# Kernel tuning notes

Measured on AMD Instinct MI355X. Metric: run time of the kernel, lower is better.

Reference implementation:

```python
import jax, jax.numpy as jnp
import numpy as np

N_EMBD = 1024
HEAD_SIZE = 64
B, T = 8, 4096


def setup_inputs() -> dict:
    key = jax.random.key(0)
    kx, kk, kq, kv = jax.random.split(key, 4)
    scale = 1.0 / np.sqrt(N_EMBD)
    x = jax.random.normal(kx, (B, T, N_EMBD), dtype=jnp.float32)
    # nn.Linear(N_EMBD, head_size, bias=False) weights, stored as [in, out] for x @ W
    W_k = jax.random.uniform(kk, (N_EMBD, HEAD_SIZE), dtype=jnp.float32, minval=-scale, maxval=scale)
    W_q = jax.random.uniform(kq, (N_EMBD, HEAD_SIZE), dtype=jnp.float32, minval=-scale, maxval=scale)
    W_v = jax.random.uniform(kv, (N_EMBD, HEAD_SIZE), dtype=jnp.float32, minval=-scale, maxval=scale)
    return {"x": x, "W_k": W_k, "W_q": W_q, "W_v": W_v}


def reference(x, W_k, W_q, W_v) -> jnp.ndarray:
    # x: [B,T,E]; projections to [B,T,H]
    k = jnp.einsum("bte,eh->bth", x, W_k)
    q = jnp.einsum("bte,eh->bth", x, W_q)
    v = jnp.einsum("bte,eh->bth", x, W_v)
    H = W_k.shape[1]
    scores = jnp.einsum("bth,bsh->bts", q, k) * (H ** -0.5)  # [B,T,T]
    Tlen = x.shape[1]
    causal = jnp.tril(jnp.ones((Tlen, Tlen), dtype=bool))
    scores = jnp.where(causal, scores, -jnp.inf)
    attn = jax.nn.softmax(scores, axis=-1)
    # dropout is identity in eval mode (deterministic reference)
    return jnp.einsum("bts,bsh->bth", attn, v)
```

## Files before the change

### kernel.cpp

```cpp
#include <hip/hip_runtime.h>
#include <hip/hip_bf16.h>
#include <math.h>


#define BB 8
#define TT 4096
#define EE 1024
#define HH 64
#define NSLOT 160
#define SLOTF 4160

typedef __attribute__((ext_vector_type(8))) short short8;
typedef __attribute__((ext_vector_type(4))) float floatx4;
typedef short8 __attribute__((may_alias)) short8_a;
typedef uint2 __attribute__((may_alias)) uint2_a;
typedef uint4 __attribute__((may_alias)) uint4_a;
typedef float4 __attribute__((may_alias)) float4_a;

#define GLDS(gp, lp)                                                     \
  __builtin_amdgcn_global_load_lds(                                      \
      (const __attribute__((address_space(1))) unsigned int*)(gp),       \
      (__attribute__((address_space(3))) unsigned int*)(lp), 16, 0, 0)

__device__ __forceinline__ unsigned short f2bf(float f) {
  union { float f; unsigned int u; } v; v.f = f;
  unsigned int r = v.u + 0x7fffu + ((v.u >> 16) & 1u);
  return (unsigned short)(r >> 16);
}
__device__ __forceinline__ unsigned int pk2(float a, float b) {
  unsigned int r;
  asm("v_cvt_pk_bf16_f32 %0, %1, %2" : "=v"(r) : "v"(a), "v"(b));
  return r;
}
__device__ __forceinline__ floatx4 fzero() {
  floatx4 z = {0.f, 0.f, 0.f, 0.f};
  return z;
}
__device__ __forceinline__ floatx4 mfma_bf16(short8 a, short8 b, floatx4 c) {
  return __builtin_amdgcn_mfma_f32_16x16x32_bf16(a, b, c, 0, 0, 0);
}
__device__ __forceinline__ short8 pack8(float4 a, float4 b) {
  union { unsigned int u[4]; short8 s; } r;
  r.u[0] = pk2(a.x, a.y);
  r.u[1] = pk2(a.z, a.w);
  r.u[2] = pk2(b.x, b.y);
  r.u[3] = pk2(b.z, b.w);
  return r.s;
}

__global__ __launch_bounds__(256) void wt_kernel(
    const float* __restrict__ Wk, const float* __restrict__ Wq,
    const float* __restrict__ Wv, unsigned short* __restrict__ wt3) {
  __shared__ float tile[64][65];
  const int m = blockIdx.y;
  const int eb = blockIdx.x;
  const float* W = (m == 0) ? Wk : ((m == 1) ? Wq : Wv);
  const int t = threadIdx.x;
  {
    const int r = t >> 2;
    const int c0 = (t & 3) * 16;
    const float* src = W + (size_t)(eb * 64 + r) * 64 + c0;
#pragma unroll
    for (int i = 0; i < 16; ++i) tile[r][c0 + i] = src[i];
  }
  __syncthreads();
  {
    const int h = t >> 2;
    const int e0 = (t & 3) * 16;
    unsigned int w[8];
#pragma unroll
    for (int i = 0; i < 8; ++i)
      w[i] = pk2(tile[e0 + 2 * i][h], tile[e0 + 2 * i + 1][h]);
    unsigned short* dst = wt3 + (size_t)(m * 64 + h) * EE + eb * 64 + e0;
    ((uint4_a*)dst)[0] = make_uint4(w[0], w[1], w[2], w[3]);
    ((uint4_a*)(dst + 8))[0] = make_uint4(w[4], w[5], w[6], w[7]);
  }
}

__global__ __launch_bounds__(256) void proj_kernel(
    const float* __restrict__ x, const unsigned short* __restrict__ wt3,
    unsigned short* __restrict__ kws, unsigned short* __restrict__ qws,
    unsigned short* __restrict__ vtws) {
  __shared__ __align__(16) unsigned char LB[3][20480];
  const int t = threadIdx.x;
  const int wv = t >> 6, lane = t & 63;
  const int l16 = lane & 15, quad = lane >> 4;
  const int mshalf = wv & 1;
  const int jbase = (wv >> 1) * 6;
  const size_t row0 = (size_t)blockIdx.x * 64;

  floatx4 acc[6][2];
#pragma unroll
  for (int j = 0; j < 6; ++j)
#pragma unroll
    for (int m2 = 0; m2 < 2; ++m2) acc[j][m2] = fzero();

  const int sg = (lane & 7) ^ ((lane >> 3) & 7);
  const int arow = lane >> 3;

#define STAGE(bufp, cc)                                                        \
  {                                                                            \
    _Pragma("unroll") for (int i = 0; i < 5; ++i) {                            \
      const int q = wv * 5 + i;                                                \
      if (q < 8) {                                                             \
        const float* gp =                                                      \
            x + (row0 + 8 * q + arow) * EE + (cc) * 32 + sg * 4;               \
        GLDS(gp, (bufp) + q * 1024);                                           \
      } else {                                                                 \
        const int j = q - 8;                                                   \
        const unsigned short* gp =                                             \
            wt3 + (size_t)(j * 16 + l16) * EE + (cc) * 32 + quad * 8;          \
        GLDS(gp, (bufp) + 8192 + j * 1024);                                    \
      }                                                                        \
    }                                                                          \
  }

  STAGE(&LB[0][0], 0);
  STAGE(&LB[1][0], 1);
  asm volatile("s_waitcnt vmcnt(5)" ::: "memory");
  __builtin_amdgcn_s_barrier();
  __builtin_amdgcn_sched_barrier(0);

  int cur = 0;
  for (int c = 0; c < 32; ++c) {
    const unsigned char* Ab = &LB[cur][0];
    float4 a4[2][2];
#pragma unroll
    for (int m2 = 0; m2 < 2; ++m2) {
      const int row = mshalf * 32 + m2 * 16 + l16;
#pragma unroll
      for (int h = 0; h < 2; ++h) {
        const int gsw = (quad * 2 + h) ^ (row & 7);
        a4[m2][h] = *(const float4_a*)(Ab + row * 128 + gsw * 16);
      }
    }
    if (c + 2 < 32) {
      int sb = cur + 2;
      if (sb >= 3) sb -= 3;
      STAGE(&LB[sb][0], c + 2);
    }
    short8 af[2];
#pragma unroll
    for (int m2 = 0; m2 < 2; ++m2) af[m2] = pack8(a4[m2][0], a4[m2][1]);
#pragma unroll
    for (int jj = 0; jj < 6; ++jj) {
      short8 bfv = *(const short8_a*)(Ab + 8192 + (size_t)(jbase + jj) * 1024 +
                                      lane * 16);
#pragma unroll
      for (int m2 = 0; m2 < 2; ++m2)
        acc[jj][m2] = mfma_bf16(af[m2], bfv, acc[jj][m2]);
    }
    if (c < 31) {
      if (c <= 29) {
        asm volatile("s_waitcnt vmcnt(5)" ::: "memory");
      } else {
        asm volatile("s_waitcnt vmcnt(0)" ::: "memory");
      }
      __builtin_amdgcn_s_barrier();
      __builtin_amdgcn_sched_barrier(0);
    }
    cur = (cur == 2) ? 0 : cur + 1;
  }
#undef STAGE

  const int b = (int)(row0 >> 12);
  const int tt0 = (int)(row0 & (TT - 1));
#pragma unroll
  for (int j = 0; j < 6; ++j) {
    const int jg = jbase + j;
    const int m = jg >> 2;
    const int h0 = (jg & 3) * 16;
#pragma unroll
    for (int m2 = 0; m2 < 2; ++m2) {
      floatx4 a = acc[j][m2];
      const int rbase = mshalf * 32 + m2 * 16 + quad * 4;
      if (m == 0) {
#pragma unroll
        for (int r = 0; r < 4; ++r)
          kws[(row0 + rbase + r) * HH + h0 + l16] = f2bf(a[r]);
      } else if (m == 1) {
#pragma unroll
        for (int r = 0; r < 4; ++r)
          qws[(row0 + rbase + r) * HH + h0 + l16] = f2bf(a[r] * 0.18033688011112042f);
      } else {
        uint2 p;
        p.x = pk2(a[0], a[1]);
        p.y = pk2(a[2], a[3]);
        ((uint2_a*)&vtws[(size_t)(b * 64 + h0 + l16) * TT + tt0 + rbase])[0] = p;
      }
    }
  }
}

template <bool SPLIT>
__global__ __launch_bounds__(256) void attn_kernel(
    const unsigned short* __restrict__ kws, const unsigned short* __restrict__ qws,
    const unsigned short* __restrict__ vtws, float* __restrict__ dst) {
  __shared__ unsigned short KV[2][16][512];
  __shared__ unsigned short pb[4][16][72];
  const int t = threadIdx.x;
  const int wv = t >> 6, lane = t & 63;
  const int l16 = lane & 15, quad = lane >> 4;
  const int id = (int)blockIdx.x;
  int b, jq, kt0, kt1;
  if (SPLIT) {
    b = id & 7;
    const int cid = id >> 3;
    int s, S;
    if (cid < 16) {
      jq = cid; s = 0; S = 1;
    } else if (cid < 48) {
      const int u = cid - 16; jq = 16 + (u >> 1); s = u & 1; S = 2;
    } else if (cid < 96) {
      const int u = cid - 48; const int d = u / 3; jq = 32 + d; s = u - 3 * d; S = 3;
    } else {
      const int u = cid - 96; jq = 48 + (u >> 2); s = u & 3; S = 4;
    }
    const int n = jq + 1;
    kt0 = (s * n) / S;
    kt1 = ((s + 1) * n) / S;
  } else {
    const int r255 = id & 255;
    b = r255 & 7;
    const int m = r255 >> 3;
    jq = (id < 256) ? m : 63 - m;
    kt0 = 0;
    kt1 = jq + 1;
  }
  const int q0 = jq * 64;
  const int qrow = q0 + wv * 16 + l16;

  const unsigned short* qp = qws + ((size_t)b * TT + qrow) * HH + quad * 8;
  short8 qa0 = *(const short8_a*)(qp);
  short8 qa1 = *(const short8_a*)(qp + 32);

  floatx4 o[4];
#pragma unroll
  for (int nt = 0; nt < 4; ++nt) o[nt] = fzero();
  float lsum = 0.f;

#define STAGE_KV(buf, ks)                                                      \
  {                                                                            \
    _Pragma("unroll") for (int i = 0; i < 4; ++i) {                            \
      const int idx = wv * 4 + i;                                              \
      const unsigned short* gp;                                                \
      if (idx < 8) {                                                           \
        const int nt = idx >> 1, f = idx & 1;                                  \
        gp = kws + ((size_t)b * TT + (ks) + nt * 16 + l16) * HH + f * 32 +     \
             quad * 8;                                                         \
      } else {                                                                 \
        const int nt = (idx - 8) >> 1, f = idx & 1;                            \
        gp = vtws + ((size_t)(b * 64 + nt * 16 + l16)) * TT + (ks) + f * 32 +  \
             quad * 8;                                                         \
      }                                                                        \
      GLDS(gp, &KV[buf][idx][0]);                                              \
    }                                                                          \
  }

  STAGE_KV(0, kt0 * 64);
  __syncthreads();

  for (int kt = kt0; kt < kt1; ++kt) {
    const int cur = (kt - kt0) & 1;
    const int ks = kt * 64;
    if (kt + 1 < kt1) STAGE_KV(cur ^ 1, ks + 64);

    floatx4 sc[4];
#pragma unroll
    for (int nt = 0; nt < 4; ++nt) {
      short8 kf0 = *(const short8_a*)&KV[cur][nt * 2][lane * 8];
      short8 kf1 = *(const short8_a*)&KV[cur][nt * 2 + 1][lane * 8];
      floatx4 z = fzero();
      z = mfma_bf16(kf0, qa0, z);
      z = mfma_bf16(kf1, qa1, z);
      sc[nt] = z;
    }
    if (kt == jq) {
#pragma unroll
      for (int nt = 0; nt < 4; ++nt)
#pragma unroll
        for (int r = 0; r < 4; ++r) {
          const int key = ks + nt * 16 + quad * 4 + r;
          if (key > qrow) sc[nt][r] = -1e30f;
        }
    }
#pragma unroll
    for (int nt = 0; nt < 4; ++nt) {
      const float p0 = exp2f(sc[nt][0]);
      const float p1 = exp2f(sc[nt][1]);
      const float p2 = exp2f(sc[nt][2]);
      const float p3 = exp2f(sc[nt][3]);
      lsum += (p0 + p1) + (p2 + p3);
      uint2 pw;
      pw.x = pk2(p0, p1);
      pw.y = pk2(p2, p3);
      ((uint2_a*)&pb[wv][l16][nt * 16 + quad * 4])[0] = pw;
    }
    short8 pf0 = *(const short8_a*)&pb[wv][l16][quad * 8];
    short8 pf1 = *(const short8_a*)&pb[wv][l16][quad * 8 + 32];
#pragma unroll
    for (int nt = 0; nt < 4; ++nt) {
      short8 vf0 = *(const short8_a*)&KV[cur][8 + nt * 2][lane * 8];
      short8 vf1 = *(const short8_a*)&KV[cur][8 + nt * 2 + 1][lane * 8];
      o[nt] = mfma_bf16(vf0, pf0, o[nt]);
      o[nt] = mfma_bf16(vf1, pf1, o[nt]);
    }
    __syncthreads();
  }
#undef STAGE_KV

  float lr = lsum;
  lr += __shfl_xor(lr, 16);
  lr += __shfl_xor(lr, 32);

  if (SPLIT) {
    float* op = dst + (size_t)id * SLOTF;
    const int ql = wv * 16 + l16;
#pragma unroll
    for (int nt = 0; nt < 4; ++nt) {
      float4 st;
      st.x = o[nt][0];
      st.y = o[nt][1];
      st.z = o[nt][2];
      st.w = o[nt][3];
      *(float4_a*)&op[(size_t)ql * 64 + nt * 16 + quad * 4] = st;
    }
    if (lane < 16) op[4096 + wv * 16 + lane] = lr;
  } else {
    const float inv = 1.0f / lr;
#pragma unroll
    for (int nt = 0; nt < 4; ++nt) {
      float4 st;
      st.x = o[nt][0] * inv;
      st.y = o[nt][1] * inv;
      st.z = o[nt][2] * inv;
      st.w = o[nt][3] * inv;
      *(float4_a*)&dst[((size_t)b * TT + qrow) * HH + nt * 16 + quad * 4] = st;
    }
  }
}

__global__ __launch_bounds__(256) void comb_kernel(
    const float* __restrict__ part, float* __restrict__ out) {
  const int id = (int)blockIdx.x;
  const int b = id & 7;
  const int jq = id >> 3;
  const int tq = jq >> 4;
  const int S = tq + 1;
  const int P = 8 * tq * (tq + 1) + (jq & 15) * S;
  const int t = threadIdx.x;
  const int r0 = t >> 6;
  const int h = t & 63;
  const float* s0 = part + (size_t)(b + 8 * P) * SLOTF;
  const size_t sstr = (size_t)8 * SLOTF;

#pragma unroll 4
  for (int i = 0; i < 16; ++i) {
    const int r = i * 4 + r0;
    float acc = 0.f, l = 0.f;
    for (int s2 = 0; s2 < S; ++s2) {
      acc += s0[(size_t)s2 * sstr + (size_t)r * 64 + h];
      l += s0[(size_t)s2 * sstr + 4096 + r];
    }
    out[((size_t)b * TT + jq * 64 + r) * HH + h] = acc / l;
  }
}

extern "C" void kernel_launch(void* const* d_in, const int* in_sizes, int n_in,
                              void* d_out, int out_size, void* d_ws, size_t ws_size,
                              hipStream_t stream) {
  const float* x = (const float*)d_in[0];
  const float* Wk = (const float*)d_in[1];
  const float* Wq = (const float*)d_in[2];
  const float* Wv = (const float*)d_in[3];
  float* out = (float*)d_out;

  unsigned short* kws = (unsigned short*)d_ws;
  unsigned short* qws = kws + (size_t)BB * TT * HH;
  unsigned short* vtws = qws + (size_t)BB * TT * HH;
  unsigned short* wt3 = vtws + (size_t)BB * TT * HH;
  float* part = (float*)(wt3 + (size_t)3 * HH * EE);

  const size_t base_bytes = (size_t)3 * BB * TT * HH * 2 + (size_t)3 * HH * EE * 2;
  const size_t need = base_bytes + (size_t)BB * NSLOT * SLOTF * 4;
  const bool use_split = (ws_size >= need);

  hipLaunchKernelGGL(wt_kernel, dim3(16, 3), dim3(256), 0, stream, Wk, Wq, Wv, wt3);
  hipLaunchKernelGGL(proj_kernel, dim3(512), dim3(256), 0, stream, x, wt3, kws, qws,
                     vtws);
  if (use_split) {
    hipLaunchKernelGGL((attn_kernel<true>), dim3(BB * NSLOT), dim3(256), 0, stream,
                       kws, qws, vtws, part);
    hipLaunchKernelGGL(comb_kernel, dim3(512), dim3(256), 0, stream, part, out);
  } else {
    hipLaunchKernelGGL((attn_kernel<false>), dim3(512), dim3(256), 0, stream,
                       kws, qws, vtws, out);
  }
}
```

Before: 283.3 us.

## Use 128-row query tiles with 8-wave blocks in split attention

Replaces the 4-wave, 64-query-row split attention kernel with an 8-wave, 128-query-row variant. Each staged K/V tile is now shared by twice as many query rows, which halves K/V global traffic and the number of staging loads per row. The split schedule drops to 80 slots per batch, and the combine kernel is adjusted to 128-row groups. In exchange there are fewer blocks, so the causal work balances more coarsely, and two diagonal tiles per block need masking.

Measured after the change: 297.2 us. 1.05x slower.

```diff
diff --git a/kernel.cpp b/kernel.cpp
--- a/kernel.cpp
+++ b/kernel.cpp
@@ -7,8 +7,8 @@
 #define TT 4096
 #define EE 1024
 #define HH 64
-#define NSLOT 160
-#define SLOTF 4160
+#define NSLOT2 80
+#define SLOTF2 8320
 
 typedef __attribute__((ext_vector_type(8))) short short8;
 typedef __attribute__((ext_vector_type(4))) float floatx4;
@@ -192,7 +192,131 @@
   }
 }
 
-template <bool SPLIT>
+__global__ __launch_bounds__(512) void attn8_kernel(
+    const unsigned short* __restrict__ kws, const unsigned short* __restrict__ qws,
+    const unsigned short* __restrict__ vtws, float* __restrict__ part) {
+  __shared__ unsigned short KV[2][16][512];
+  __shared__ unsigned short pb[8][16][72];
+  const int t = threadIdx.x;
+  const int wv = t >> 6, lane = t & 63;
+  const int l16 = lane & 15, quad = lane >> 4;
+  const int id = (int)blockIdx.x;
+  const int b = id & 7;
+  const int cid = id >> 3;
+  int jq, s, S;
+  if (cid < 8) {
+    jq = cid; s = 0; S = 1;
+  } else if (cid < 24) {
+    const int u = cid - 8; jq = 8 + (u >> 1); s = u & 1; S = 2;
+  } else if (cid < 48) {
+    const int u = cid - 24; const int d = u / 3; jq = 16 + d; s = u - 3 * d; S = 3;
+  } else {
+    const int u = cid - 48; jq = 24 + (u >> 2); s = u & 3; S = 4;
+  }
+  const int n = 2 * (jq + 1);
+  const int kt0 = (s * n) / S;
+  const int kt1 = ((s + 1) * n) / S;
+  const int dt0 = 2 * jq;
+  const int q0 = jq * 128;
+  const int qrow = q0 + wv * 16 + l16;
+
+  const unsigned short* qp = qws + ((size_t)b * TT + qrow) * HH + quad * 8;
+  short8 qa0 = *(const short8_a*)(qp);
+  short8 qa1 = *(const short8_a*)(qp + 32);
+
+  floatx4 o[4];
+#pragma unroll
+  for (int nt = 0; nt < 4; ++nt) o[nt] = fzero();
+  float lsum = 0.f;
+
+#define STAGE_KV8(buf, ks)                                                     \
+  {                                                                            \
+    _Pragma("unroll") for (int i = 0; i < 2; ++i) {                            \
+      const int idx = wv * 2 + i;                                              \
+      const unsigned short* gp;                                                \
+      if (idx < 8) {                                                           \
+        const int nt = idx >> 1, f = idx & 1;                                  \
+        gp = kws + ((size_t)b * TT + (ks) + nt * 16 + l16) * HH + f * 32 +     \
+             quad * 8;                                                         \
+      } else {                                                                 \
+        const int nt = (idx - 8) >> 1, f = idx & 1;                            \
+        gp = vtws + ((size_t)(b * 64 + nt * 16 + l16)) * TT + (ks) + f * 32 +  \
+             quad * 8;                                                         \
+      }                                                                        \
+      GLDS(gp, &KV[buf][idx][0]);                                              \
+    }                                                                          \
+  }
+
+  STAGE_KV8(0, kt0 * 64);
+  __syncthreads();
+
+  for (int kt = kt0; kt < kt1; ++kt) {
+    const int cur = (kt - kt0) & 1;
+    const int ks = kt * 64;
+    if (kt + 1 < kt1) STAGE_KV8(cur ^ 1, ks + 64);
+
+    floatx4 sc[4];
+#pragma unroll
+    for (int nt = 0; nt < 4; ++nt) {
+      short8 kf0 = *(const short8_a*)&KV[cur][nt * 2][lane * 8];
+      short8 kf1 = *(const short8_a*)&KV[cur][nt * 2 + 1][lane * 8];
+      floatx4 z = fzero();
+      z = mfma_bf16(kf0, qa0, z);
+      z = mfma_bf16(kf1, qa1, z);
+      sc[nt] = z;
+    }
+    if (kt >= dt0) {
+#pragma unroll
+      for (int nt = 0; nt < 4; ++nt)
+#pragma unroll
+        for (int r = 0; r < 4; ++r) {
+          const int key = ks + nt * 16 + quad * 4 + r;
+          if (key > qrow) sc[nt][r] = -1e30f;
+        }
+    }
+#pragma unroll
+    for (int nt = 0; nt < 4; ++nt) {
+      const float p0 = exp2f(sc[nt][0]);
+      const float p1 = exp2f(sc[nt][1]);
+      const float p2 = exp2f(sc[nt][2]);
+      const float p3 = exp2f(sc[nt][3]);
+      lsum += (p0 + p1) + (p2 + p3);
+      uint2 pw;
+      pw.x = pk2(p0, p1);
+      pw.y = pk2(p2, p3);
+      ((uint2_a*)&pb[wv][l16][nt * 16 + quad * 4])[0] = pw;
+    }
+    short8 pf0 = *(const short8_a*)&pb[wv][l16][quad * 8];
+    short8 pf1 = *(const short8_a*)&pb[wv][l16][quad * 8 + 32];
+#pragma unroll
+    for (int nt = 0; nt < 4; ++nt) {
+      short8 vf0 = *(const short8_a*)&KV[cur][8 + nt * 2][lane * 8];
+      short8 vf1 = *(const short8_a*)&KV[cur][8 + nt * 2 + 1][lane * 8];
+      o[nt] = mfma_bf16(vf0, pf0, o[nt]);
+      o[nt] = mfma_bf16(vf1, pf1, o[nt]);
+    }
+    __syncthreads();
+  }
+#undef STAGE_KV8
+
+  float lr = lsum;
+  lr += __shfl_xor(lr, 16);
+  lr += __shfl_xor(lr, 32);
+
+  float* op = part + (size_t)id * SLOTF2;
+  const int ql = wv * 16 + l16;
+#pragma unroll
+  for (int nt = 0; nt < 4; ++nt) {
+    float4 st;
+    st.x = o[nt][0];
+    st.y = o[nt][1];
+    st.z = o[nt][2];
+    st.w = o[nt][3];
+    *(float4_a*)&op[(size_t)ql * 64 + nt * 16 + quad * 4] = st;
+  }
+  if (lane < 16) op[8192 + wv * 16 + lane] = lr;
+}
+
 __global__ __launch_bounds__(256) void attn_kernel(
     const unsigned short* __restrict__ kws, const unsigned short* __restrict__ qws,
     const unsigned short* __restrict__ vtws, float* __restrict__ dst) {
@@ -202,31 +326,11 @@
   const int wv = t >> 6, lane = t & 63;
   const int l16 = lane & 15, quad = lane >> 4;
   const int id = (int)blockIdx.x;
-  int b, jq, kt0, kt1;
-  if (SPLIT) {
-    b = id & 7;
-    const int cid = id >> 3;
-    int s, S;
-    if (cid < 16) {
-      jq = cid; s = 0; S = 1;
-    } else if (cid < 48) {
-      const int u = cid - 16; jq = 16 + (u >> 1); s = u & 1; S = 2;
-    } else if (cid < 96) {
-      const int u = cid - 48; const int d = u / 3; jq = 32 + d; s = u - 3 * d; S = 3;
-    } else {
-      const int u = cid - 96; jq = 48 + (u >> 2); s = u & 3; S = 4;
-    }
-    const int n = jq + 1;
-    kt0 = (s * n) / S;
-    kt1 = ((s + 1) * n) / S;
-  } else {
-    const int r255 = id & 255;
-    b = r255 & 7;
-    const int m = r255 >> 3;
-    jq = (id < 256) ? m : 63 - m;
-    kt0 = 0;
-    kt1 = jq + 1;
-  }
+  const int r255 = id & 255;
+  const int b = r255 & 7;
+  const int m = r255 >> 3;
+  const int jq = (id < 256) ? m : 63 - m;
+  const int kt1 = jq + 1;
   const int q0 = jq * 64;
   const int qrow = q0 + wv * 16 + l16;
 
@@ -257,11 +361,11 @@
     }                                                                          \
   }
 
-  STAGE_KV(0, kt0 * 64);
+  STAGE_KV(0, 0);
   __syncthreads();
 
-  for (int kt = kt0; kt < kt1; ++kt) {
-    const int cur = (kt - kt0) & 1;
+  for (int kt = 0; kt < kt1; ++kt) {
+    const int cur = kt & 1;
     const int ks = kt * 64;
     if (kt + 1 < kt1) STAGE_KV(cur ^ 1, ks + 64);
 
@@ -312,31 +416,15 @@
   float lr = lsum;
   lr += __shfl_xor(lr, 16);
   lr += __shfl_xor(lr, 32);
-
-  if (SPLIT) {
-    float* op = dst + (size_t)id * SLOTF;
-    const int ql = wv * 16 + l16;
-#pragma unroll
-    for (int nt = 0; nt < 4; ++nt) {
-      float4 st;
-      st.x = o[nt][0];
-      st.y = o[nt][1];
-      st.z = o[nt][2];
-      st.w = o[nt][3];
-      *(float4_a*)&op[(size_t)ql * 64 + nt * 16 + quad * 4] = st;
-    }
-    if (lane < 16) op[4096 + wv * 16 + lane] = lr;
-  } else {
-    const float inv = 1.0f / lr;
-#pragma unroll
-    for (int nt = 0; nt < 4; ++nt) {
-      float4 st;
-      st.x = o[nt][0] * inv;
-      st.y = o[nt][1] * inv;
-      st.z = o[nt][2] * inv;
-      st.w = o[nt][3] * inv;
-      *(float4_a*)&dst[((size_t)b * TT + qrow) * HH + nt * 16 + quad * 4] = st;
-    }
+  const float inv = 1.0f / lr;
+#pragma unroll
+  for (int nt = 0; nt < 4; ++nt) {
+    float4 st;
+    st.x = o[nt][0] * inv;
+    st.y = o[nt][1] * inv;
+    st.z = o[nt][2] * inv;
+    st.w = o[nt][3] * inv;
+    *(float4_a*)&dst[((size_t)b * TT + qrow) * HH + nt * 16 + quad * 4] = st;
   }
 }
 
@@ -345,24 +433,24 @@
   const int id = (int)blockIdx.x;
   const int b = id & 7;
   const int jq = id >> 3;
-  const int tq = jq >> 4;
-  const int S = tq + 1;
-  const int P = 8 * tq * (tq + 1) + (jq & 15) * S;
+  const int g = jq >> 3;
+  const int S = g + 1;
+  const int P = 4 * g * (g + 1) + (jq & 7) * S;
   const int t = threadIdx.x;
   const int r0 = t >> 6;
   const int h = t & 63;
-  const float* s0 = part + (size_t)(b + 8 * P) * SLOTF;
-  const size_t sstr = (size_t)8 * SLOTF;
+  const float* s0 = part + (size_t)(b + 8 * P) * SLOTF2;
+  const size_t sstr = (size_t)8 * SLOTF2;
 
 #pragma unroll 4
-  for (int i = 0; i < 16; ++i) {
+  for (int i = 0; i < 32; ++i) {
     const int r = i * 4 + r0;
     float acc = 0.f, l = 0.f;
     for (int s2 = 0; s2 < S; ++s2) {
       acc += s0[(size_t)s2 * sstr + (size_t)r * 64 + h];
-      l += s0[(size_t)s2 * sstr + 4096 + r];
-    }
-    out[((size_t)b * TT + jq * 64 + r) * HH + h] = acc / l;
+      l += s0[(size_t)s2 * sstr + 8192 + r];
+    }
+    out[((size_t)b * TT + jq * 128 + r) * HH + h] = acc / l;
   }
 }
 
@@ -382,18 +470,18 @@
   float* part = (float*)(wt3 + (size_t)3 * HH * EE);
 
   const size_t base_bytes = (size_t)3 * BB * TT * HH * 2 + (size_t)3 * HH * EE * 2;
-  const size_t need = base_bytes + (size_t)BB * NSLOT * SLOTF * 4;
+  const size_t need = base_bytes + (size_t)BB * NSLOT2 * SLOTF2 * 4;
   const bool use_split = (ws_size >= need);
 
   hipLaunchKernelGGL(wt_kernel, dim3(16, 3), dim3(256), 0, stream, Wk, Wq, Wv, wt3);
   hipLaunchKernelGGL(proj_kernel, dim3(512), dim3(256), 0, stream, x, wt3, kws, qws,
                      vtws);
   if (use_split) {
-    hipLaunchKernelGGL((attn_kernel<true>), dim3(BB * NSLOT), dim3(256), 0, stream,
+    hipLaunchKernelGGL(attn8_kernel, dim3(BB * NSLOT2), dim3(512), 0, stream,
                        kws, qws, vtws, part);
-    hipLaunchKernelGGL(comb_kernel, dim3(512), dim3(256), 0, stream, part, out);
+    hipLaunchKernelGGL(comb_kernel, dim3(256), dim3(256), 0, stream, part, out);
   } else {
-    hipLaunchKernelGGL((attn_kernel<false>), dim3(512), dim3(256), 0, stream,
+    hipLaunchKernelGGL(attn_kernel, dim3(512), dim3(256), 0, stream,
                        kws, qws, vtws, out);
   }
 }
```

## Halve projection tile rows, double grid, switch to simple double buffering

Applied to the files above, without the earlier changes.

Projection blocks now cover 32 rows instead of 64, and the grid doubles to 1024 blocks. Each wave owns 3 of the 12 output column tiles over all 32 rows, so the A tile is shared across all waves. The triple-buffer pipeline with explicit vmcnt waits becomes a two-stage double buffer with __syncthreads, cutting LDS per block. The aim is more blocks and occupancy to hide x-load latency, at the cost of reloading the weight slab twice as often and a shallower prefetch pipeline.

Measured after the change: 310.0 us. 9.4% more time.

```diff
diff --git a/kernel.cpp b/kernel.cpp
--- a/kernel.cpp
+++ b/kernel.cpp
@@ -81,17 +81,16 @@
     const float* __restrict__ x, const unsigned short* __restrict__ wt3,
     unsigned short* __restrict__ kws, unsigned short* __restrict__ qws,
     unsigned short* __restrict__ vtws) {
-  __shared__ __align__(16) unsigned char LB[3][20480];
+  __shared__ __align__(16) unsigned char LB[2][16384];
   const int t = threadIdx.x;
   const int wv = t >> 6, lane = t & 63;
   const int l16 = lane & 15, quad = lane >> 4;
-  const int mshalf = wv & 1;
-  const int jbase = (wv >> 1) * 6;
-  const size_t row0 = (size_t)blockIdx.x * 64;
-
-  floatx4 acc[6][2];
-#pragma unroll
-  for (int j = 0; j < 6; ++j)
+  const int jbase = wv * 3;
+  const size_t row0 = (size_t)blockIdx.x * 32;
+
+  floatx4 acc[3][2];
+#pragma unroll
+  for (int j = 0; j < 3; ++j)
 #pragma unroll
     for (int m2 = 0; m2 < 2; ++m2) acc[j][m2] = fzero();
 
@@ -100,80 +99,65 @@
 
 #define STAGE(bufp, cc)                                                        \
   {                                                                            \
-    _Pragma("unroll") for (int i = 0; i < 5; ++i) {                            \
-      const int q = wv * 5 + i;                                                \
-      if (q < 8) {                                                             \
+    _Pragma("unroll") for (int i = 0; i < 4; ++i) {                            \
+      const int q = wv * 4 + i;                                                \
+      if (q < 4) {                                                             \
         const float* gp =                                                      \
             x + (row0 + 8 * q + arow) * EE + (cc) * 32 + sg * 4;               \
         GLDS(gp, (bufp) + q * 1024);                                           \
       } else {                                                                 \
-        const int j = q - 8;                                                   \
+        const int j = q - 4;                                                   \
         const unsigned short* gp =                                             \
             wt3 + (size_t)(j * 16 + l16) * EE + (cc) * 32 + quad * 8;          \
-        GLDS(gp, (bufp) + 8192 + j * 1024);                                    \
+        GLDS(gp, (bufp) + 4096 + j * 1024);                                    \
       }                                                                        \
     }                                                                          \
   }
 
   STAGE(&LB[0][0], 0);
-  STAGE(&LB[1][0], 1);
-  asm volatile("s_waitcnt vmcnt(5)" ::: "memory");
-  __builtin_amdgcn_s_barrier();
-  __builtin_amdgcn_sched_barrier(0);
-
-  int cur = 0;
+  __syncthreads();
+
   for (int c = 0; c < 32; ++c) {
+    const int cur = c & 1;
+    if (c < 31) STAGE(&LB[cur ^ 1][0], c + 1);
+
     const unsigned char* Ab = &LB[cur][0];
     float4 a4[2][2];
 #pragma unroll
     for (int m2 = 0; m2 < 2; ++m2) {
-      const int row = mshalf * 32 + m2 * 16 + l16;
+      const int row = m2 * 16 + l16;
 #pragma unroll
       for (int h = 0; h < 2; ++h) {
         const int gsw = (quad * 2 + h) ^ (row & 7);
         a4[m2][h] = *(const float4_a*)(Ab + row * 128 + gsw * 16);
       }
     }
-    if (c + 2 < 32) {
-      int sb = cur + 2;
-      if (sb >= 3) sb -= 3;
-      STAGE(&LB[sb][0], c + 2);
-    }
     short8 af[2];
 #pragma unroll
     for (int m2 = 0; m2 < 2; ++m2) af[m2] = pack8(a4[m2][0], a4[m2][1]);
 #pragma unroll
-    for (int jj = 0; jj < 6; ++jj) {
-      short8 bfv = *(const short8_a*)(Ab + 8192 + (size_t)(jbase + jj) * 1024 +
+    for (int jj = 0; jj < 3; ++jj) {
+      short8 bfv = *(const short8_a*)(Ab + 4096 + (size_t)(jbase + jj) * 1024 +
                                       lane * 16);
 #pragma unroll
       for (int m2 = 0; m2 < 2; ++m2)
         acc[jj][m2] = mfma_bf16(af[m2], bfv, acc[jj][m2]);
     }
-    if (c < 31) {
-      if (c <= 29) {
-        asm volatile("s_waitcnt vmcnt(5)" ::: "memory");
-      } else {
-        asm volatile("s_waitcnt vmcnt(0)" ::: "memory");
-      }
-      __builtin_amdgcn_s_barrier();
-      __builtin_amdgcn_sched_barrier(0);
-    }
-    cur = (cur == 2) ? 0 : cur + 1;
+    __syncthreads();
   }
 #undef STAGE
 
   const int b = (int)(row0 >> 12);
   const int tt0 = (int)(row0 & (TT - 1));
 #pragma unroll
-  for (int j = 0; j < 6; ++j) {
+  for (int j = 0; j < 3; ++j) {
     const int jg = jbase + j;
     const int m = jg >> 2;
     const int h0 = (jg & 3) * 16;
 #pragma unroll
     for (int m2 = 0; m2 < 2; ++m2) {
       floatx4 a = acc[j][m2];
-      const int rbase = mshalf * 32 + m2 * 16 + quad * 4;
+      const int rbase = m2 * 16 + quad * 4;
       if (m == 0) {
 #pragma unroll
         for (int r = 0; r < 4; ++r)
@@ -386,7 +370,7 @@
   const bool use_split = (ws_size >= need);
 
   hipLaunchKernelGGL(wt_kernel, dim3(16, 3), dim3(256), 0, stream, Wk, Wq, Wv, wt3);
-  hipLaunchKernelGGL(proj_kernel, dim3(512), dim3(256), 0, stream, x, wt3, kws, qws,
+  hipLaunchKernelGGL(proj_kernel, dim3(1024), dim3(256), 0, stream, x, wt3, kws, qws,
                      vtws);
   if (use_split) {
     hipLaunchKernelGGL((attn_kernel<true>), dim3(BB * NSLOT), dim3(256), 0, stream,
```
